# Performance work log

Hardware: AMD Instinct MI355X
Metric: run time of the kernel (lower is better)

## Reference

```python
import jax, jax.numpy as jnp
import numpy as np
from jax import lax

B_, L_ = 4, 512
D_MODEL, N_LAYER = 384, 4
D_INNER, N_STATE, DT_RANK, D_CONV = 768, 16, 24, 4
VOCAB, FEAT = 1544, 1536


def setup_inputs() -> dict:
    key = jax.random.key(0)
    ks = iter(jax.random.split(key, 32))
    nrm = lambda shape, s=0.02: jax.random.normal(next(ks), shape, jnp.float32) * s
    input_ids = jax.random.normal(next(ks), (B_, L_, VOCAB), jnp.float32)
    return dict(
        input_ids=input_ids,
        fc_W=nrm((D_MODEL, VOCAB)), fc_b=jnp.zeros((D_MODEL,), jnp.float32),
        in_proj_W=nrm((N_LAYER, 2 * D_INNER, D_MODEL)),
        conv_W=nrm((N_LAYER, D_INNER, 1, D_CONV), 0.2),
        conv_b=jnp.zeros((N_LAYER, D_INNER), jnp.float32),
        x_proj_W=nrm((N_LAYER, DT_RANK + 2 * N_STATE, D_INNER)),
        dt_proj_W=nrm((N_LAYER, D_INNER, DT_RANK)),
        dt_proj_b=jnp.zeros((N_LAYER, D_INNER), jnp.float32),
        A_log=jnp.tile(jnp.log(jnp.arange(1, N_STATE + 1, dtype=jnp.float32)), (N_LAYER, D_INNER, 1)),
        D=jnp.ones((N_LAYER, D_INNER), jnp.float32),
        out_proj_W=nrm((N_LAYER, D_MODEL, D_INNER)),
        norm_W=jnp.ones((N_LAYER, D_MODEL), jnp.float32),
        normf_W=jnp.ones((D_MODEL,), jnp.float32),
        head_W=nrm((FEAT, D_MODEL)),
    )


def _rmsnorm(x, w, eps=1e-5):
    return x * lax.rsqrt(jnp.mean(x * x, axis=-1, keepdims=True) + eps) * w


def _selective_scan(u, delta, A, B, C, D):
    # u, delta: (b, l, d); A: (d, n); B, C: (b, l, n); D: (d,)
    dA = jnp.exp(jnp.einsum('bld,dn->bldn', delta, A))          # (b, l, d, n)
    dBu = jnp.einsum('bld,bln->bldn', delta * u, B)             # (b, l, d, n)
    b, l, d = u.shape
    n = A.shape[1]

    def step(h, inp):
        dA_t, dBu_t, c_t = inp                                   # (b,d,n),(b,d,n),(b,n)
        h = dA_t * h + dBu_t
        y = jnp.einsum('bdn,bn->bd', h, c_t)
        return h, y

    h0 = jnp.zeros((b, d, n), u.dtype)
    _, ys = lax.scan(step, h0, (dA.transpose(1, 0, 2, 3), dBu.transpose(1, 0, 2, 3), C.transpose(1, 0, 2)))
    return ys.transpose(1, 0, 2) + u * D                         # (b, l, d)


def _mamba(input_ids, fc_W, fc_b, in_proj_W, conv_W, conv_b, x_proj_W,
           dt_proj_W, dt_proj_b, A_log, D, out_proj_W, norm_W, normf_W, head_W):
    x = input_ids @ fc_W.T + fc_b                                # (b, l, d_model)
    for i in range(N_LAYER):
        h = _rmsnorm(x, norm_W[i])
        xz = h @ in_proj_W[i].T                                  # (b, l, 2*d_inner)
        xc, res = jnp.split(xz, 2, axis=-1)
        xc = xc.transpose(0, 2, 1)                               # (b, d_inner, l)
        xc = lax.conv_general_dilated(
            xc, conv_W[i], window_strides=(1,), padding=[(D_CONV - 1, 0)],
            feature_group_count=D_INNER, dimension_numbers=('NCH', 'OIH', 'NCH'))
        xc = xc + conv_b[i][None, :, None]
        u = jax.nn.silu(xc.transpose(0, 2, 1))                   # (b, l, d_inner)
        x_dbl = u @ x_proj_W[i].T
        delta, Bm, Cm = jnp.split(x_dbl, [DT_RANK, DT_RANK + N_STATE], axis=-1)
        delta = jax.nn.softplus(delta @ dt_proj_W[i].T + dt_proj_b[i])
        A = -jnp.exp(A_log[i])
        y = _selective_scan(u, delta, A, Bm, Cm, D[i])
        y = y * jax.nn.silu(res)
        x = y @ out_proj_W[i].T + x                              # residual
    x = _rmsnorm(x, normf_W)
    return x @ head_W.T                                          # (b, l, feat)


def reference(input_ids, fc_W, fc_b, in_proj_W, conv_W, conv_b, x_proj_W,
              dt_proj_W, dt_proj_b, A_log, D, out_proj_W, norm_W, normf_W, head_W):
    return _mamba(input_ids, fc_W, fc_b, in_proj_W, conv_W, conv_b, x_proj_W,
                  dt_proj_W, dt_proj_b, A_log, D, out_proj_W, norm_W, normf_W, head_W)
```

## Files before the change

### kernel.cpp

```cpp
#include <hip/hip_runtime.h>
#include <math.h>

#define B_ 4
#define L_ 512
#define MROWS 2048
#define D_MODEL 384
#define N_LAYER 4
#define D_INNER 768
#define N_STATE 16
#define DT_RANK 24
#define D_CONV 4
#define VOCAB 1544
#define FEAT 1536
#define XPROJ_N 56
#define NCH 16
#define SCH 32
#define DG 2

typedef __attribute__((ext_vector_type(8))) short short8;
typedef __attribute__((ext_vector_type(4))) float floatx4;

__device__ __forceinline__ float softplus_f(float x) { return x > 20.f ? x : log1pf(expf(x)); }
__device__ __forceinline__ float silu_f(float x) { return x / (1.f + __expf(-x)); }

__device__ __forceinline__ unsigned pack2bf(float x, float y) {
    unsigned ux = __float_as_uint(x); ux = (ux + 0x7FFFu + ((ux >> 16) & 1u)) >> 16;
    unsigned uy = __float_as_uint(y); uy = (uy + 0x7FFFu + ((uy >> 16) & 1u)) >> 16;
    return ux | (uy << 16);
}

template <int CTRL>
__device__ __forceinline__ float dpp_radd(float x) {
    int r = __builtin_amdgcn_update_dpp(0, __float_as_int(x), CTRL, 0xf, 0xf, true);
    return x + __int_as_float(r);
}

__device__ __forceinline__ void wave_lds_fence() {
    asm volatile("s_waitcnt lgkmcnt(0)" ::: "memory");
    __builtin_amdgcn_wave_barrier();
}

__device__ __forceinline__ float4 ld4_guard(const float* __restrict__ p, int k, int ke) {
    if (k + 3 < ke) return *(const float4*)(p + k);
    float4 r = make_float4(0.f, 0.f, 0.f, 0.f);
    if (k + 0 < ke) r.x = p[k + 0];
    if (k + 1 < ke) r.y = p[k + 1];
    if (k + 2 < ke) r.z = p[k + 2];
    return r;
}

__device__ __forceinline__ short8 ld8h_guard(const short* __restrict__ p, int k, int ke) {
    if (k + 7 < ke) return *(const short8*)(p + k);
    short8 r = {0, 0, 0, 0, 0, 0, 0, 0};
#pragma unroll
    for (int j = 0; j < 8; ++j)
        if (k + j < ke) r[j] = p[k + j];
    return r;
}

struct CastDesc {
    const float* src[6];
    short*       dst[6];
    unsigned     cum[6];
};

__global__ __launch_bounds__(256) void cast_w_k(CastDesc cd, unsigned total4,
                                                float4* __restrict__ zb, unsigned z4)
{
    unsigned i = blockIdx.x * 256 + threadIdx.x;
    if (i < total4) {
        int s = 0;
#pragma unroll
        for (int j = 0; j < 5; ++j)
            if (i >= cd.cum[j] && s == j) s = j + 1;
        unsigned off = i - (s ? cd.cum[s - 1] : 0u);
        float4 v = ((const float4*)cd.src[s])[off];
        uint2 pk;
        pk.x = pack2bf(v.x, v.y);
        pk.y = pack2bf(v.z, v.w);
        ((uint2*)cd.dst[s])[off] = pk;
    } else {
        unsigned zi = i - total4;
        if (zi < z4) zb[zi] = make_float4(0.f, 0.f, 0.f, 0.f);
    }
}

__global__ __launch_bounds__(256) void rmsnorm_cast_k(
    const float* __restrict__ x, const float* __restrict__ nw,
    unsigned* __restrict__ outp)
{
    const int idx = blockIdx.x * 256 + threadIdx.x;
    const int row = idx >> 3, q = idx & 7;
    const float* xr = x + (size_t)row * D_MODEL + q * 48;
    float4 v[12];
    float s = 0.f;
#pragma unroll
    for (int i = 0; i < 12; ++i) {
        v[i] = *(const float4*)(xr + i * 4);
        s += v[i].x * v[i].x + v[i].y * v[i].y + v[i].z * v[i].z + v[i].w * v[i].w;
    }
    s += __shfl_xor(s, 1, 64);
    s += __shfl_xor(s, 2, 64);
    s += __shfl_xor(s, 4, 64);
    const float sc = rsqrtf(s / (float)D_MODEL + 1e-5f);
    unsigned* op = outp + ((size_t)row * D_MODEL + q * 48) / 2;
#pragma unroll
    for (int i = 0; i < 12; ++i) {
        float4 wv = *(const float4*)(nw + q * 48 + i * 4);
        op[i * 2]     = pack2bf(v[i].x * (sc * wv.x), v[i].y * (sc * wv.y));
        op[i * 2 + 1] = pack2bf(v[i].z * (sc * wv.z), v[i].w * (sc * wv.w));
    }
}

#define ASTR 40

template <int EPI, bool ATOMIC, bool NG, bool ABF>
__global__ __launch_bounds__(256) void mfma_gemm(
    const float* __restrict__ A, const short* __restrict__ Abf,
    const short* __restrict__ Wb,
    const float* __restrict__ bias,
    float* __restrict__ C, int M, int N, int K, int lda, int ldc, int KC)
{
    __shared__ short As[2][64 * ASTR];
    __shared__ short Ws[2][64 * ASTR];

    const int t  = threadIdx.x;
    const int m0 = blockIdx.y * 64;
    const int n0 = blockIdx.x * 64;
    const int ks = blockIdx.z * KC;
    const int ke = min(K, ks + KC);

    const int srow = t >> 2;
    const int sseg = (t & 3) * 8;

    float4 ra0, ra1;
    short8 ra8, rw8;

    auto prefetch = [&](int k0) {
        if (ABF) {
            ra8 = ld8h_guard(Abf + (size_t)(m0 + srow) * lda, k0 + sseg, ke);
        } else {
            const float* ar = A + (size_t)(m0 + srow) * lda;
            ra0 = ld4_guard(ar, k0 + sseg, ke);
            ra1 = ld4_guard(ar, k0 + sseg + 4, ke);
        }
        if (!NG || (n0 + srow) < N) {
            rw8 = ld8h_guard(Wb + (size_t)(n0 + srow) * (size_t)K, k0 + sseg, ke);
        } else {
            rw8 = (short8){0, 0, 0, 0, 0, 0, 0, 0};
        }
    };

    auto stage = [&](int p) {
        if (ABF) {
            *(short8*)&As[p][srow * ASTR + sseg] = ra8;
        } else {
            int4 pa;
            pa.x = pack2bf(ra0.x, ra0.y); pa.y = pack2bf(ra0.z, ra0.w);
            pa.z = pack2bf(ra1.x, ra1.y); pa.w = pack2bf(ra1.z, ra1.w);
            *(int4*)&As[p][srow * ASTR + sseg] = pa;
        }
        *(short8*)&Ws[p][srow * ASTR + sseg] = rw8;
    };

    prefetch(ks);
    stage(0);
    if (ks + 32 < ke) prefetch(ks + 32);
    __syncthreads();

    floatx4 acc[2][2];
#pragma unroll
    for (int i = 0; i < 2; ++i)
#pragma unroll
        for (int j = 0; j < 2; ++j) acc[i][j] = (floatx4){0.f, 0.f, 0.f, 0.f};

    const int w    = t >> 6;
    const int lane = t & 63;
    const int quad = lane >> 4;
    const int lm   = lane & 15;
    const int aoff = ((w >> 1) * 32 + lm) * ASTR + quad * 8;
    const int boff = ((w & 1) * 32 + lm) * ASTR + quad * 8;

    int p = 0;
    for (int k0 = ks; k0 < ke; k0 += 32) {
        const bool more = (k0 + 32 < ke);
        if (more) {
            stage(p ^ 1);
            if (k0 + 64 < ke) prefetch(k0 + 64);
        }
        short8 a0 = *(const short8*)&As[p][aoff];
        short8 a1 = *(const short8*)&As[p][aoff + 16 * ASTR];
        short8 b0 = *(const short8*)&Ws[p][boff];
        short8 b1 = *(const short8*)&Ws[p][boff + 16 * ASTR];
        acc[0][0] = __builtin_amdgcn_mfma_f32_16x16x32_bf16(a0, b0, acc[0][0], 0, 0, 0);
        acc[0][1] = __builtin_amdgcn_mfma_f32_16x16x32_bf16(a0, b1, acc[0][1], 0, 0, 0);
        acc[1][0] = __builtin_amdgcn_mfma_f32_16x16x32_bf16(a1, b0, acc[1][0], 0, 0, 0);
        acc[1][1] = __builtin_amdgcn_mfma_f32_16x16x32_bf16(a1, b1, acc[1][1], 0, 0, 0);
        if (more) {
            __syncthreads();
            p ^= 1;
        }
    }

    const int rbase = m0 + (w >> 1) * 32 + quad * 4;
    const int cbase = n0 + (w & 1) * 32 + lm;
#pragma unroll
    for (int mt = 0; mt < 2; ++mt)
#pragma unroll
        for (int nt = 0; nt < 2; ++nt) {
            const int gc = cbase + nt * 16;
            if (NG && gc >= N) continue;
#pragma unroll
            for (int r = 0; r < 4; ++r) {
                const size_t gr = rbase + mt * 16 + r;
                float v = acc[mt][nt][r];
                if (ATOMIC) {
                    if (EPI == 1 && blockIdx.z == 0) v += bias[gc];
                    atomicAdd(&C[gr * ldc + gc], v);
                } else {
                    if (EPI == 1) v += bias[gc];
                    if (EPI == 2) v = softplus_f(v + bias[gc]);
                    C[gr * ldc + gc] = v;
                }
            }
        }
}

__global__ __launch_bounds__(256) void conv_silu_k(
    const float* __restrict__ xz, const float* __restrict__ w,
    const float* __restrict__ cb, float* __restrict__ u, short* __restrict__ ubf)
{
    int idx = blockIdx.x * 256 + threadIdx.x;
    if (idx >= MROWS * (D_INNER / 4)) return;
    int dq = idx % (D_INNER / 4);
    int m  = idx / (D_INNER / 4);
    int d0 = dq * 4;
    int b = m / L_, l = m % L_;
    float4 wq[4];
#pragma unroll
    for (int j = 0; j < 4; ++j) wq[j] = *(const float4*)(w + (d0 + j) * D_CONV);
    float acc[4];
#pragma unroll
    for (int j = 0; j < 4; ++j) acc[j] = cb[d0 + j];
#pragma unroll
    for (int tt = 0; tt < 4; ++tt) {
        int ll = l - 3 + tt;
        if (ll >= 0) {
            float4 xv = *(const float4*)(xz + (size_t)(b * L_ + ll) * (2 * D_INNER) + d0);
            acc[0] = fmaf(xv.x, ((const float*)&wq[0])[tt], acc[0]);
            acc[1] = fmaf(xv.y, ((const float*)&wq[1])[tt], acc[1]);
            acc[2] = fmaf(xv.z, ((const float*)&wq[2])[tt], acc[2]);
            acc[3] = fmaf(xv.w, ((const float*)&wq[3])[tt], acc[3]);
        }
    }
    float4 o = make_float4(silu_f(acc[0]), silu_f(acc[1]), silu_f(acc[2]), silu_f(acc[3]));
    *(float4*)(u + (size_t)m * D_INNER + d0) = o;
    uint2 pk;
    pk.x = pack2bf(o.x, o.y);
    pk.y = pack2bf(o.z, o.w);
    *(uint2*)(ubf + (size_t)m * D_INNER + d0) = pk;
}

__global__ __launch_bounds__(512, 4) void scan_fused_k(
    const float* __restrict__ xdbl, const float* __restrict__ u,
    const float* __restrict__ xz,
    const float* __restrict__ dtW, const float* __restrict__ dtb,
    const float* __restrict__ A_log, const float* __restrict__ Dp,
    short* __restrict__ ybf)
{
    __shared__ __align__(16) float2 sdu[NCH][SCH][DG];
    __shared__ __align__(16) float  sy[NCH][SCH][DG];
    __shared__ __align__(16) float2 sPH[NCH][DG][16];

    const int t  = threadIdx.x;
    const int w  = t >> 6;
    const int l  = t & 63;
    const int ch = l >> 5;
    const int c  = w * 2 + ch;
    const int dl = (l >> 4) & 1;
    const int n  = l & 15;
    const int bx  = blockIdx.x;
    const int dgi = (bx & 7) * (D_INNER / DG / 8) + (bx >> 3);
    const int d0 = dgi * DG;
    const int d  = d0 + dl;
    const int b  = blockIdx.y;

    const int tc = t >> 5, tj = t & 31;
    const size_t trow = (size_t)b * L_ + t;

    float2 rv  = *(const float2*)(xz + trow * (2 * D_INNER) + D_INNER + d0);
    float2 uv2 = *(const float2*)(u + trow * D_INNER + d0);

    {
        const float* wd = dtW + (size_t)d0 * DT_RANK;
        const float* xr = xdbl + trow * XPROJ_N;
        float acc0 = dtb[d0];
        float acc1 = dtb[d0 + 1];
#pragma unroll
        for (int q = 0; q < 6; ++q) {
            float4 xv = *(const float4*)(xr + q * 4);
            float4 w0 = *(const float4*)(wd + q * 4);
            float4 w1 = *(const float4*)(wd + DT_RANK + q * 4);
            acc0 = fmaf(xv.x, w0.x, acc0); acc0 = fmaf(xv.y, w0.y, acc0);
            acc0 = fmaf(xv.z, w0.z, acc0); acc0 = fmaf(xv.w, w0.w, acc0);
            acc1 = fmaf(xv.x, w1.x, acc1); acc1 = fmaf(xv.y, w1.y, acc1);
            acc1 = fmaf(xv.z, w1.z, acc1); acc1 = fmaf(xv.w, w1.w, acc1);
        }
        float4 pk = make_float4(softplus_f(acc0), uv2.x, softplus_f(acc1), uv2.y);
        *(float4*)&sdu[tc][tj][0] = pk;
    }
    wave_lds_fence();

    const float Av = -expf(A_log[d * N_STATE + n]);
    const float Dd = Dp[d];
    const float* xbn = xdbl + ((size_t)b * L_ + c * SCH) * XPROJ_N + DT_RANK + n;

    {
        float h = 0.f, sdv = 0.f;
        float rB[8];
#pragma unroll
        for (int q = 0; q < 8; ++q) rB[q] = xbn[q * XPROJ_N];
#pragma unroll
        for (int g = 0; g < SCH / 8; ++g) {
            float nB[8];
            if (g + 1 < SCH / 8) {
#pragma unroll
                for (int q = 0; q < 8; ++q) nB[q] = xbn[(g * 8 + 8 + q) * XPROJ_N];
            }
#pragma unroll
            for (int q = 0; q < 8; ++q) {
                const int j = g * 8 + q;
                float2 du = *(const float2*)&sdu[c][j][dl];
                float e  = __expf(du.x * Av);
                h = fmaf(e, h, du.x * du.y * rB[q]);
                sdv += du.x;
            }
#pragma unroll
            for (int q = 0; q < 8; ++q) rB[q] = nB[q];
        }
        float2 ph;
        ph.x = __expf(sdv * Av);
        ph.y = h;
        *(float2*)&sPH[c][dl][n] = ph;
    }

    float rB[8], rC[8];
#pragma unroll
    for (int q = 0; q < 8; ++q) {
        rB[q] = xbn[q * XPROJ_N];
        rC[q] = xbn[q * XPROJ_N + N_STATE];
    }
    __syncthreads();

    float hs = 0.f;
#pragma unroll
    for (int s = 0; s < NCH - 1; ++s) {
        float2 ph = *(const float2*)&sPH[s][dl][n];
        const bool m = s < c;
        hs = fmaf(m ? ph.x : 1.f, hs, m ? ph.y : 0.f);
    }

    {
        float h = hs;
#pragma unroll
        for (int g = 0; g < SCH / 8; ++g) {
            float nB[8], nC[8];
            if (g + 1 < SCH / 8) {
#pragma unroll
                for (int q = 0; q < 8; ++q) {
                    nB[q] = xbn[(g * 8 + 8 + q) * XPROJ_N];
                    nC[q] = xbn[(g * 8 + 8 + q) * XPROJ_N + N_STATE];
                }
            }
#pragma unroll
            for (int q = 0; q < 8; ++q) {
                const int j = g * 8 + q;
                float2 du = *(const float2*)&sdu[c][j][dl];
                float e  = __expf(du.x * Av);
                h = fmaf(e, h, du.x * du.y * rB[q]);
                float p = h * rC[q];
                p = dpp_radd<0x128>(p);
                p = dpp_radd<0x124>(p);
                p = dpp_radd<0x122>(p);
                p = dpp_radd<0x121>(p);
                if (n == 0) sy[c][j][dl] = fmaf(du.y, Dd, p);
            }
#pragma unroll
            for (int q = 0; q < 8; ++q) { rB[q] = nB[q]; rC[q] = nC[q]; }
        }
    }
    wave_lds_fence();

    {
        float2 yv = *(const float2*)&sy[tc][tj][0];
        float o0 = yv.x * silu_f(rv.x);
        float o1 = yv.y * silu_f(rv.y);
        *(unsigned*)(ybf + trow * D_INNER + d0) = pack2bf(o0, o1);
    }
}

extern "C" void kernel_launch(void* const* d_in, const int* in_sizes, int n_in,
                              void* d_out, int out_size, void* d_ws, size_t ws_size,
                              hipStream_t stream)
{
    const float* input_ids = (const float*)d_in[0];
    const float* fc_W      = (const float*)d_in[1];
    const float* fc_b      = (const float*)d_in[2];
    const float* in_proj_W = (const float*)d_in[3];
    const float* conv_W    = (const float*)d_in[4];
    const float* conv_b    = (const float*)d_in[5];
    const float* x_proj_W  = (const float*)d_in[6];
    const float* dt_proj_W = (const float*)d_in[7];
    const float* dt_proj_b = (const float*)d_in[8];
    const float* A_log     = (const float*)d_in[9];
    const float* Dp        = (const float*)d_in[10];
    const float* out_proj_W= (const float*)d_in[11];
    const float* norm_W    = (const float*)d_in[12];
    const float* normf_W   = (const float*)d_in[13];
    const float* head_W    = (const float*)d_in[14];
    float* out = (float*)d_out;

    float* ws       = (float*)d_ws;
    float* x_ws     = ws;
    float* xdbl_ws  = x_ws    + (size_t)MROWS * D_MODEL;
    float* xz_ws    = xdbl_ws + (size_t)N_LAYER * MROWS * XPROJ_N;
    float* u_ws     = xz_ws   + (size_t)MROWS * 2 * D_INNER;
    short* bf       = (short*)(u_ws + (size_t)MROWS * D_INNER);
    short* wbf_fc   = bf;
    short* wbf_in   = wbf_fc  + (size_t)D_MODEL * VOCAB;
    short* wbf_x    = wbf_in  + (size_t)N_LAYER * 2 * D_INNER * D_MODEL;
    short* wbf_out  = wbf_x   + (size_t)N_LAYER * XPROJ_N * D_INNER;
    short* wbf_head = wbf_out + (size_t)N_LAYER * D_MODEL * D_INNER;
    short* ids_bf   = wbf_head+ (size_t)FEAT * D_MODEL;
    short* ubf_ws   = ids_bf  + (size_t)MROWS * VOCAB;
    short* ybf_ws   = ubf_ws  + (size_t)MROWS * D_INNER;
    short* xnorm_bf = ybf_ws  + (size_t)MROWS * D_INNER;

    const dim3 blk(256);
    const dim3 blk512(512);

    CastDesc cd;
    cd.src[0] = fc_W;       cd.dst[0] = wbf_fc;
    cd.src[1] = in_proj_W;  cd.dst[1] = wbf_in;
    cd.src[2] = x_proj_W;   cd.dst[2] = wbf_x;
    cd.src[3] = out_proj_W; cd.dst[3] = wbf_out;
    cd.src[4] = head_W;     cd.dst[4] = wbf_head;
    cd.src[5] = input_ids;  cd.dst[5] = ids_bf;
    unsigned c0 = (unsigned)(D_MODEL * VOCAB / 4);
    unsigned c1 = c0 + (unsigned)(N_LAYER * 2 * D_INNER * D_MODEL / 4);
    unsigned c2 = c1 + (unsigned)(N_LAYER * XPROJ_N * D_INNER / 4);
    unsigned c3 = c2 + (unsigned)(N_LAYER * D_MODEL * D_INNER / 4);
    unsigned c4 = c3 + (unsigned)(FEAT * D_MODEL / 4);
    unsigned c5 = c4 + (unsigned)(MROWS * VOCAB / 4);
    cd.cum[0] = c0; cd.cum[1] = c1; cd.cum[2] = c2;
    cd.cum[3] = c3; cd.cum[4] = c4; cd.cum[5] = c5;
    const unsigned zero4 = (unsigned)((MROWS * D_MODEL + N_LAYER * MROWS * XPROJ_N) / 4);
    cast_w_k<<<(c5 + zero4 + 255) / 256, blk, 0, stream>>>(cd, c5, (float4*)x_ws, zero4);

    mfma_gemm<1, true, false, true><<<dim3(D_MODEL / 64, MROWS / 64, 7), blk, 0, stream>>>(
        nullptr, ids_bf, wbf_fc, fc_b, x_ws,
        MROWS, D_MODEL, VOCAB, VOCAB, D_MODEL, 256);

    for (int i = 0; i < N_LAYER; ++i) {
        float* xdbl_i = xdbl_ws + (size_t)i * MROWS * XPROJ_N;

        rmsnorm_cast_k<<<MROWS * 8 / 256, blk, 0, stream>>>(
            x_ws, norm_W + i * D_MODEL, (unsigned*)xnorm_bf);

        mfma_gemm<0, false, false, true><<<dim3(2 * D_INNER / 64, MROWS / 64, 1), blk, 0, stream>>>(
            nullptr, xnorm_bf, wbf_in + (size_t)i * 2 * D_INNER * D_MODEL,
            nullptr, xz_ws,
            MROWS, 2 * D_INNER, D_MODEL, D_MODEL, 2 * D_INNER, D_MODEL);

        conv_silu_k<<<(MROWS * (D_INNER / 4) + 255) / 256, blk, 0, stream>>>(
            xz_ws, conv_W + (size_t)i * D_INNER * D_CONV, conv_b + i * D_INNER,
            u_ws, ubf_ws);

        mfma_gemm<0, true, true, true><<<dim3(1, MROWS / 64, 6), blk, 0, stream>>>(
            nullptr, ubf_ws, wbf_x + (size_t)i * XPROJ_N * D_INNER,
            nullptr, xdbl_i,
            MROWS, XPROJ_N, D_INNER, D_INNER, XPROJ_N, 128);

        scan_fused_k<<<dim3(D_INNER / DG, B_), blk512, 0, stream>>>(
            xdbl_i, u_ws, xz_ws,
            dt_proj_W + (size_t)i * D_INNER * DT_RANK, dt_proj_b + i * D_INNER,
            A_log + (size_t)i * D_INNER * N_STATE, Dp + i * D_INNER, ybf_ws);

        mfma_gemm<0, true, false, true><<<dim3(D_MODEL / 64, MROWS / 64, 2), blk, 0, stream>>>(
            nullptr, ybf_ws, wbf_out + (size_t)i * D_MODEL * D_INNER,
            nullptr, x_ws,
            MROWS, D_MODEL, D_INNER, D_INNER, D_MODEL, 384);
    }

    rmsnorm_cast_k<<<MROWS * 8 / 256, blk, 0, stream>>>(
        x_ws, normf_W, (unsigned*)xnorm_bf);
    mfma_gemm<0, false, false, true><<<dim3(FEAT / 64, MROWS / 64, 1), blk, 0, stream>>>(
        nullptr, xnorm_bf, wbf_head, nullptr, out,
        MROWS, FEAT, D_MODEL, D_MODEL, FEAT, D_MODEL);
}
```

Baseline: 428.5 us.

## Fuse depthwise conv+SiLU into x_proj GEMM A-load and scan kernel

Removes the standalone conv_silu kernel and its u/ubf intermediate buffers. The x_proj GEMM now computes the causal depthwise conv and SiLU while staging its A tile from xz, and the scan kernel recomputes u for its own channels directly from xz. This saves one launch per layer and a write plus re-read of u, at the cost of redundant conv arithmetic and four-tap loads done in both consumers.

```diff
diff --git a/kernel.cpp b/kernel.cpp
--- a/kernel.cpp
+++ b/kernel.cpp
@@ -40,15 +40,6 @@
     __builtin_amdgcn_wave_barrier();
 }
 
-__device__ __forceinline__ float4 ld4_guard(const float* __restrict__ p, int k, int ke) {
-    if (k + 3 < ke) return *(const float4*)(p + k);
-    float4 r = make_float4(0.f, 0.f, 0.f, 0.f);
-    if (k + 0 < ke) r.x = p[k + 0];
-    if (k + 1 < ke) r.y = p[k + 1];
-    if (k + 2 < ke) r.z = p[k + 2];
-    return r;
-}
-
 __device__ __forceinline__ short8 ld8h_guard(const short* __restrict__ p, int k, int ke) {
     if (k + 7 < ke) return *(const short8*)(p + k);
     short8 r = {0, 0, 0, 0, 0, 0, 0, 0};
@@ -114,11 +105,12 @@
 
 #define ASTR 40
 
-template <int EPI, bool ATOMIC, bool NG, bool ABF>
+template <int EPI, bool ATOMIC, bool NG, bool ABF, bool CONV>
 __global__ __launch_bounds__(256) void mfma_gemm(
     const float* __restrict__ A, const short* __restrict__ Abf,
     const short* __restrict__ Wb,
     const float* __restrict__ bias,
+    const float* __restrict__ cw, const float* __restrict__ cbp,
     float* __restrict__ C, int M, int N, int K, int lda, int ldc, int KC)
 {
     __shared__ short As[2][64 * ASTR];
@@ -133,16 +125,28 @@
     const int srow = t >> 2;
     const int sseg = (t & 3) * 8;
 
-    float4 ra0, ra1;
     short8 ra8, rw8;
+    float4 tapA[4], tapB[4];
+    int pk_k = 0;
 
     auto prefetch = [&](int k0) {
-        if (ABF) {
+        if (CONV) {
+            pk_k = k0;
+            const int m = m0 + srow, bb = m >> 9, l = m & 511;
+            const float* base = A + (size_t)(bb << 9) * (2 * D_INNER) + (k0 + sseg);
+#pragma unroll
+            for (int tt = 0; tt < 4; ++tt) {
+                const int ll = l - 3 + tt;
+                if (ll >= 0) {
+                    tapA[tt] = *(const float4*)(base + (size_t)ll * (2 * D_INNER));
+                    tapB[tt] = *(const float4*)(base + (size_t)ll * (2 * D_INNER) + 4);
+                } else {
+                    tapA[tt] = make_float4(0.f, 0.f, 0.f, 0.f);
+                    tapB[tt] = make_float4(0.f, 0.f, 0.f, 0.f);
+                }
+            }
+        } else if (ABF) {
             ra8 = ld8h_guard(Abf + (size_t)(m0 + srow) * lda, k0 + sseg, ke);
-        } else {
-            const float* ar = A + (size_t)(m0 + srow) * lda;
-            ra0 = ld4_guard(ar, k0 + sseg, ke);
-            ra1 = ld4_guard(ar, k0 + sseg + 4, ke);
         }
         if (!NG || (n0 + srow) < N) {
             rw8 = ld8h_guard(Wb + (size_t)(n0 + srow) * (size_t)K, k0 + sseg, ke);
@@ -152,13 +156,35 @@
     };
 
     auto stage = [&](int p) {
-        if (ABF) {
+        if (CONV) {
+            const int kk = pk_k + sseg;
+            float accv[8];
+#pragma unroll
+            for (int j = 0; j < 8; ++j) accv[j] = cbp[kk + j];
+#pragma unroll
+            for (int j = 0; j < 4; ++j) {
+                float4 wj = *(const float4*)(cw + (size_t)(kk + j) * 4);
+                accv[j] = fmaf(((const float*)&tapA[0])[j], wj.x, accv[j]);
+                accv[j] = fmaf(((const float*)&tapA[1])[j], wj.y, accv[j]);
+                accv[j] = fmaf(((const float*)&tapA[2])[j], wj.z, accv[j]);
+                accv[j] = fmaf(((const float*)&tapA[3])[j], wj.w, accv[j]);
+            }
+#pragma unroll
+            for (int j = 0; j < 4; ++j) {
+                float4 wj = *(const float4*)(cw + (size_t)(kk + 4 + j) * 4);
+                accv[4 + j] = fmaf(((const float*)&tapB[0])[j], wj.x, accv[4 + j]);
+                accv[4 + j] = fmaf(((const float*)&tapB[1])[j], wj.y, accv[4 + j]);
+                accv[4 + j] = fmaf(((const float*)&tapB[2])[j], wj.z, accv[4 + j]);
+                accv[4 + j] = fmaf(((const float*)&tapB[3])[j], wj.w, accv[4 + j]);
+            }
+            int4 pa;
+            pa.x = pack2bf(silu_f(accv[0]), silu_f(accv[1]));
+            pa.y = pack2bf(silu_f(accv[2]), silu_f(accv[3]));
+            pa.z = pack2bf(silu_f(accv[4]), silu_f(accv[5]));
+            pa.w = pack2bf(silu_f(accv[6]), silu_f(accv[7]));
+            *(int4*)&As[p][srow * ASTR + sseg] = pa;
+        } else {
             *(short8*)&As[p][srow * ASTR + sseg] = ra8;
-        } else {
-            int4 pa;
-            pa.x = pack2bf(ra0.x, ra0.y); pa.y = pack2bf(ra0.z, ra0.w);
-            pa.z = pack2bf(ra1.x, ra1.y); pa.w = pack2bf(ra1.z, ra1.w);
-            *(int4*)&As[p][srow * ASTR + sseg] = pa;
         }
         *(short8*)&Ws[p][srow * ASTR + sseg] = rw8;
     };
@@ -226,44 +252,9 @@
         }
 }
 
-__global__ __launch_bounds__(256) void conv_silu_k(
-    const float* __restrict__ xz, const float* __restrict__ w,
-    const float* __restrict__ cb, float* __restrict__ u, short* __restrict__ ubf)
-{
-    int idx = blockIdx.x * 256 + threadIdx.x;
-    if (idx >= MROWS * (D_INNER / 4)) return;
-    int dq = idx % (D_INNER / 4);
-    int m  = idx / (D_INNER / 4);
-    int d0 = dq * 4;
-    int b = m / L_, l = m % L_;
-    float4 wq[4];
-#pragma unroll
-    for (int j = 0; j < 4; ++j) wq[j] = *(const float4*)(w + (d0 + j) * D_CONV);
-    float acc[4];
-#pragma unroll
-    for (int j = 0; j < 4; ++j) acc[j] = cb[d0 + j];
-#pragma unroll
-    for (int tt = 0; tt < 4; ++tt) {
-        int ll = l - 3 + tt;
-        if (ll >= 0) {
-            float4 xv = *(const float4*)(xz + (size_t)(b * L_ + ll) * (2 * D_INNER) + d0);
-            acc[0] = fmaf(xv.x, ((const float*)&wq[0])[tt], acc[0]);
-            acc[1] = fmaf(xv.y, ((const float*)&wq[1])[tt], acc[1]);
-            acc[2] = fmaf(xv.z, ((const float*)&wq[2])[tt], acc[2]);
-            acc[3] = fmaf(xv.w, ((const float*)&wq[3])[tt], acc[3]);
-        }
-    }
-    float4 o = make_float4(silu_f(acc[0]), silu_f(acc[1]), silu_f(acc[2]), silu_f(acc[3]));
-    *(float4*)(u + (size_t)m * D_INNER + d0) = o;
-    uint2 pk;
-    pk.x = pack2bf(o.x, o.y);
-    pk.y = pack2bf(o.z, o.w);
-    *(uint2*)(ubf + (size_t)m * D_INNER + d0) = pk;
-}
-
 __global__ __launch_bounds__(512, 4) void scan_fused_k(
-    const float* __restrict__ xdbl, const float* __restrict__ u,
-    const float* __restrict__ xz,
+    const float* __restrict__ xdbl, const float* __restrict__ xz,
+    const float* __restrict__ cw, const float* __restrict__ cbp,
     const float* __restrict__ dtW, const float* __restrict__ dtb,
     const float* __restrict__ A_log, const float* __restrict__ Dp,
     short* __restrict__ ybf)
@@ -288,8 +279,26 @@
     const int tc = t >> 5, tj = t & 31;
     const size_t trow = (size_t)b * L_ + t;
 
-    float2 rv  = *(const float2*)(xz + trow * (2 * D_INNER) + D_INNER + d0);
-    float2 uv2 = *(const float2*)(u + trow * D_INNER + d0);
+    float2 rv = *(const float2*)(xz + trow * (2 * D_INNER) + D_INNER + d0);
+
+    float2 uv2;
+    {
+        float4 w0 = *(const float4*)(cw + (size_t)d0 * 4);
+        float4 w1 = *(const float4*)(cw + (size_t)(d0 + 1) * 4);
+        float a0 = cbp[d0], a1 = cbp[d0 + 1];
+        const float* xb0 = xz + (size_t)b * L_ * (2 * D_INNER) + d0;
+#pragma unroll
+        for (int tt = 0; tt < 4; ++tt) {
+            const int ll = t - 3 + tt;
+            if (ll >= 0) {
+                float2 xv = *(const float2*)(xb0 + (size_t)ll * (2 * D_INNER));
+                a0 = fmaf(xv.x, ((const float*)&w0)[tt], a0);
+                a1 = fmaf(xv.y, ((const float*)&w1)[tt], a1);
+            }
+        }
+        uv2.x = silu_f(a0);
+        uv2.y = silu_f(a1);
+    }
 
     {
         const float* wd = dtW + (size_t)d0 * DT_RANK;
@@ -424,16 +433,14 @@
     float* x_ws     = ws;
     float* xdbl_ws  = x_ws    + (size_t)MROWS * D_MODEL;
     float* xz_ws    = xdbl_ws + (size_t)N_LAYER * MROWS * XPROJ_N;
-    float* u_ws     = xz_ws   + (size_t)MROWS * 2 * D_INNER;
-    short* bf       = (short*)(u_ws + (size_t)MROWS * D_INNER);
+    short* bf       = (short*)(xz_ws + (size_t)MROWS * 2 * D_INNER);
     short* wbf_fc   = bf;
     short* wbf_in   = wbf_fc  + (size_t)D_MODEL * VOCAB;
     short* wbf_x    = wbf_in  + (size_t)N_LAYER * 2 * D_INNER * D_MODEL;
     short* wbf_out  = wbf_x   + (size_t)N_LAYER * XPROJ_N * D_INNER;
     short* wbf_head = wbf_out + (size_t)N_LAYER * D_MODEL * D_INNER;
     short* ids_bf   = wbf_head+ (size_t)FEAT * D_MODEL;
-    short* ubf_ws   = ids_bf  + (size_t)MROWS * VOCAB;
-    short* ybf_ws   = ubf_ws  + (size_t)MROWS * D_INNER;
+    short* ybf_ws   = ids_bf  + (size_t)MROWS * VOCAB;
     short* xnorm_bf = ybf_ws  + (size_t)MROWS * D_INNER;
 
     const dim3 blk(256);
@@ -457,44 +464,42 @@
     const unsigned zero4 = (unsigned)((MROWS * D_MODEL + N_LAYER * MROWS * XPROJ_N) / 4);
     cast_w_k<<<(c5 + zero4 + 255) / 256, blk, 0, stream>>>(cd, c5, (float4*)x_ws, zero4);
 
-    mfma_gemm<1, true, false, true><<<dim3(D_MODEL / 64, MROWS / 64, 7), blk, 0, stream>>>(
-        nullptr, ids_bf, wbf_fc, fc_b, x_ws,
+    mfma_gemm<1, true, false, true, false><<<dim3(D_MODEL / 64, MROWS / 64, 7), blk, 0, stream>>>(
+        nullptr, ids_bf, wbf_fc, fc_b, nullptr, nullptr, x_ws,
         MROWS, D_MODEL, VOCAB, VOCAB, D_MODEL, 256);
 
     for (int i = 0; i < N_LAYER; ++i) {
         float* xdbl_i = xdbl_ws + (size_t)i * MROWS * XPROJ_N;
+        const float* cw_i = conv_W + (size_t)i * D_INNER * D_CONV;
+        const float* cb_i = conv_b + i * D_INNER;
 
         rmsnorm_cast_k<<<MROWS * 8 / 256, blk, 0, stream>>>(
             x_ws, norm_W + i * D_MODEL, (unsigned*)xnorm_bf);
 
-        mfma_gemm<0, false, false, true><<<dim3(2 * D_INNER / 64, MROWS / 64, 1), blk, 0, stream>>>(
+        mfma_gemm<0, false, false, true, false><<<dim3(2 * D_INNER / 64, MROWS / 64, 1), blk, 0, stream>>>(
             nullptr, xnorm_bf, wbf_in + (size_t)i * 2 * D_INNER * D_MODEL,
-            nullptr, xz_ws,
+            nullptr, nullptr, nullptr, xz_ws,
             MROWS, 2 * D_INNER, D_MODEL, D_MODEL, 2 * D_INNER, D_MODEL);
 
-        conv_silu_k<<<(MROWS * (D_INNER / 4) + 255) / 256, blk, 0, stream>>>(
-            xz_ws, conv_W + (size_t)i * D_INNER * D_CONV, conv_b + i * D_INNER,
-            u_ws, ubf_ws);
-
-        mfma_gemm<0, true, true, true><<<dim3(1, MROWS / 64, 6), blk, 0, stream>>>(
-            nullptr, ubf_ws, wbf_x + (size_t)i * XPROJ_N * D_INNER,
-            nullptr, xdbl_i,
-            MROWS, XPROJ_N, D_INNER, D_INNER, XPROJ_N, 128);
+        mfma_gemm<0, true, true, false, true><<<dim3(1, MROWS / 64, 6), blk, 0, stream>>>(
+            xz_ws, nullptr, wbf_x + (size_t)i * XPROJ_N * D_INNER,
+            nullptr, cw_i, cb_i, xdbl_i,
+            MROWS, XPROJ_N, D_INNER, 2 * D_INNER, XPROJ_N, 128);
 
         scan_fused_k<<<dim3(D_INNER / DG, B_), blk512, 0, stream>>>(
-            xdbl_i, u_ws, xz_ws,
+            xdbl_i, xz_ws, cw_i, cb_i,
             dt_proj_W + (size_t)i * D_INNER * DT_RANK, dt_proj_b + i * D_INNER,
             A_log + (size_t)i * D_INNER * N_STATE, Dp + i * D_INNER, ybf_ws);
 
-        mfma_gemm<0, true, false, true><<<dim3(D_MODEL / 64, MROWS / 64, 2), blk, 0, stream>>>(
+        mfma_gemm<0, true, false, true, false><<<dim3(D_MODEL / 64, MROWS / 64, 2), blk, 0, stream>>>(
             nullptr, ybf_ws, wbf_out + (size_t)i * D_MODEL * D_INNER,
-            nullptr, x_ws,
+            nullptr, nullptr, nullptr, x_ws,
             MROWS, D_MODEL, D_INNER, D_INNER, D_MODEL, 384);
     }
 
     rmsnorm_cast_k<<<MROWS * 8 / 256, blk, 0, stream>>>(
         x_ws, normf_W, (unsigned*)xnorm_bf);
-    mfma_gemm<0, false, false, true><<<dim3(FEAT / 64, MROWS / 64, 1), blk, 0, stream>>>(
-        nullptr, xnorm_bf, wbf_head, nullptr, out,
+    mfma_gemm<0, false, false, true, false><<<dim3(FEAT / 64, MROWS / 64, 1), blk, 0, stream>>>(
+        nullptr, xnorm_bf, wbf_head, nullptr, nullptr, nullptr, out,
         MROWS, FEAT, D_MODEL, D_MODEL, FEAT, D_MODEL);
 }
```

Result: slower. 450.0 us (+5.0%).
